# Kernel optimization log

Hardware: AMD Instinct MI355X
Metric: run time of the kernel (lower is better)

## Reference

```python
import math
import jax, jax.numpy as jnp
import numpy as np

B, S, D, H = 1, 4096, 1024, 16
HD = D // H


def setup_inputs() -> dict:
    key = jax.random.key(0)
    ks = jax.random.split(key, 11)
    s = 0.02
    inp = {
        "q": jax.random.normal(ks[0], (B, S, D), jnp.float32),
        "k": jax.random.normal(ks[1], (B, S, D), jnp.float32),
        "v": jax.random.normal(ks[2], (B, S, D), jnp.float32),
        # causal boolean mask, broadcastable over [B, H, S, S]
        "mask": jnp.tril(jnp.ones((S, S), jnp.bool_))[None, None],
        "Wq": jax.random.normal(ks[3], (D, D), jnp.float32) * s,
        "bq": jnp.zeros((D,), jnp.float32),
        "Wk": jax.random.normal(ks[4], (D, D), jnp.float32) * s,
        "bk": jnp.zeros((D,), jnp.float32),
        "Wv": jax.random.normal(ks[5], (D, D), jnp.float32) * s,
        "bv": jnp.zeros((D,), jnp.float32),
        "Wo": jax.random.normal(ks[6], (D, D), jnp.float32) * s,
        "bo": jnp.zeros((D,), jnp.float32),
    }
    return inp


def reference(q, k, v, mask, Wq, bq, Wk, bk, Wv, bv, Wo, bo):
    # projections (torch Linear: x @ W.T + b; here W is stored already transposed)
    qp = (q @ Wq + bq).reshape(B, S, H, HD)
    kp = (k @ Wk + bk).reshape(B, S, H, HD)
    vp = (v @ Wv + bv).reshape(B, S, H, HD)
    # scores: [B, H, S, S]
    scores = jnp.einsum("bqhd,bkhd->bhqk", qp, kp) / math.sqrt(HD)
    scores = jnp.where(mask, scores, -jnp.inf)
    attn = jax.nn.softmax(scores, axis=-1)
    # context: [B, H, S, HD] -> [B, S, D]
    ctx = jnp.einsum("bhqk,bkhd->bqhd", attn, vp).reshape(B, S, D)
    return ctx @ Wo + bo
```

## Files before the change

kernel.cpp:

```cpp
#include <hip/hip_runtime.h>
#include <hip/hip_bf16.h>


#define S_LEN 4096
#define D_DIM 1024
#define NHEAD 16
#define HDIM  64

typedef __hip_bfloat16 bf16;
typedef __attribute__((ext_vector_type(8))) short bf16x8v;
typedef __attribute__((ext_vector_type(4))) float f32x4;
typedef __attribute__((ext_vector_type(2))) unsigned int u32x2;

#define MFMA16(a, b, c) __builtin_amdgcn_mfma_f32_16x16x32_bf16((a), (b), (c), 0, 0, 0)

#if __has_builtin(__builtin_amdgcn_exp2f)
#define EXP2F(x) __builtin_amdgcn_exp2f(x)
#else
#define EXP2F(x) exp2f(x)
#endif

#define QSCALE (0.125f * 1.4426950408889634f)

template<int N> struct IC { static constexpr int value = N; };

__device__ __forceinline__ void async_cp16(const void* g, void* l) {
    __builtin_amdgcn_global_load_lds(
        (const __attribute__((address_space(1))) unsigned int*)g,
        (__attribute__((address_space(3))) unsigned int*)l, 16, 0, 0);
}

__device__ __forceinline__ unsigned int cvtpk_bf16(float lo, float hi) {
    unsigned int r;
    asm("v_cvt_pk_bf16_f32 %0, %1, %2" : "=v"(r) : "v"(lo), "v"(hi));
    return r;
}

__global__ __launch_bounds__(256) void cvt_bf16_k(
    const float* __restrict__ x0, const float* __restrict__ x1,
    const float* __restrict__ x2,
    bf16* __restrict__ y0, bf16* __restrict__ y1, bf16* __restrict__ y2)
{
    const float* x = (blockIdx.z == 0) ? x0 : (blockIdx.z == 1) ? x1 : x2;
    bf16*       y = (blockIdx.z == 0) ? y0 : (blockIdx.z == 1) ? y1 : y2;
    const size_t i = ((size_t)blockIdx.x * 256 + threadIdx.x);
    const float4 v = ((const float4*)x)[i];
    union { bf16 h[4]; short4 s; } u;
    u.h[0] = __float2bfloat16(v.x);
    u.h[1] = __float2bfloat16(v.y);
    u.h[2] = __float2bfloat16(v.z);
    u.h[3] = __float2bfloat16(v.w);
    ((short4*)y)[i] = u.s;
}

__global__ __launch_bounds__(256) void transpose_cvt_k(
    const float* __restrict__ W0, const float* __restrict__ W1,
    const float* __restrict__ W2, const float* __restrict__ W3,
    bf16* __restrict__ T0, bf16* __restrict__ T1,
    bf16* __restrict__ T2, bf16* __restrict__ T3)
{
    const float* W = (blockIdx.z == 0) ? W0 : (blockIdx.z == 1) ? W1
                   : (blockIdx.z == 2) ? W2 : W3;
    bf16*       Wt = (blockIdx.z == 0) ? T0 : (blockIdx.z == 1) ? T1
                   : (blockIdx.z == 2) ? T2 : T3;
    __shared__ float t[32][33];
    const int bx = blockIdx.x << 5, by = blockIdx.y << 5;
    const int tx = threadIdx.x & 31, ty = threadIdx.x >> 5;
#pragma unroll
    for (int i = 0; i < 32; i += 8)
        t[ty + i][tx] = W[(size_t)(by + ty + i) * D_DIM + bx + tx];
    __syncthreads();
#pragma unroll
    for (int i = 0; i < 32; i += 8)
        Wt[(size_t)(bx + ty + i) * D_DIM + by + tx] = __float2bfloat16(t[tx][ty + i]);
}

struct GemmJob {
    const bf16* A; const bf16* Wt; const float* bias; void* out;
    int mode; float scale;
};

__global__ __launch_bounds__(256) void gemm_k(GemmJob j0, GemmJob j1, GemmJob j2)
{
    const GemmJob j = (blockIdx.z == 0) ? j0 : (blockIdx.z == 1) ? j1 : j2;
    const int K = D_DIM;

    const int nx  = gridDim.x;
    const int lin = blockIdx.y * nx + blockIdx.x;
    const int per = (nx * gridDim.y) >> 3;
    const int bmn = (lin & 7) * per + (lin >> 3);
    const int bn = (bmn % nx) << 6;
    const int bm = (bmn / nx) << 7;

    const int tid = threadIdx.x;
    const int w = tid >> 6, lane = tid & 63;
    const int col = lane & 15, g = lane >> 4;
    const int wr = (w >> 1) << 6, wc = (w & 1) << 5;

    __shared__ bf16 As[2][128 * 64];
    __shared__ bf16 Bs[2][64 * 64];

    f32x4 acc[4][2];
#pragma unroll
    for (int i = 0; i < 4; ++i)
#pragma unroll
        for (int jj = 0; jj < 2; ++jj) acc[i][jj] = (f32x4){0.f, 0.f, 0.f, 0.f};

    auto stage = [&](int buf, int kb) {
#pragma unroll
        for (int e = 0; e < 4; ++e) {
            const int l2 = (e << 8) + tid;
            const int row = l2 >> 3, kc = l2 & 7;
            async_cp16(j.A + (size_t)(bm + row) * K + kb + (kc << 3), &As[buf][l2 << 3]);
        }
#pragma unroll
        for (int e = 0; e < 2; ++e) {
            const int l2 = (e << 8) + tid;
            const int row = l2 >> 3, kc = l2 & 7;
            async_cp16(j.Wt + (size_t)(bn + row) * K + kb + (kc << 3), &Bs[buf][l2 << 3]);
        }
    };

    stage(0, 0);
    __syncthreads();
    int cur = 0;

    for (int kb = 0; kb < K; kb += 64) {
        if (kb + 64 < K) stage(cur ^ 1, kb + 64);

#pragma unroll
        for (int s = 0; s < 2; ++s) {
            bf16x8v af[4], bfv[2];
#pragma unroll
            for (int i = 0; i < 4; ++i)
                af[i] = *(const bf16x8v*)&As[cur][((wr + (i << 4) + col) << 6) + (s << 5) + (g << 3)];
#pragma unroll
            for (int jj = 0; jj < 2; ++jj)
                bfv[jj] = *(const bf16x8v*)&Bs[cur][((wc + (jj << 4) + col) << 6) + (s << 5) + (g << 3)];
#pragma unroll
            for (int i = 0; i < 4; ++i)
#pragma unroll
                for (int jj = 0; jj < 2; ++jj)
                    acc[i][jj] = MFMA16(af[i], bfv[jj], acc[i][jj]);
        }

        __syncthreads();
        cur ^= 1;
    }

#pragma unroll
    for (int i = 0; i < 4; ++i)
#pragma unroll
    for (int jj = 0; jj < 2; ++jj)
#pragma unroll
    for (int reg = 0; reg < 4; ++reg) {
        const int row = bm + wr + (i << 4) + (g << 2) + reg;
        const int cg  = bn + wc + (jj << 4) + col;
        const float vv = (acc[i][jj][reg] + j.bias[cg]) * j.scale;
        if (j.mode == 0)
            ((bf16*)j.out)[(((size_t)(cg >> 6)) * S_LEN + row) * HDIM + (cg & 63)] =
                __float2bfloat16(vv);
        else if (j.mode == 2)
            ((bf16*)j.out)[((size_t)(cg >> 6) * HDIM + (cg & 63)) * S_LEN + row] =
                __float2bfloat16(vv);
        else
            ((float*)j.out)[(size_t)row * D_DIM + cg] = vv;
    }
}

__global__ __launch_bounds__(256) void attn_mfma_k(
    const bf16* __restrict__ Qp, const bf16* __restrict__ Kp,
    const bf16* __restrict__ Vt, bf16* __restrict__ ctx,
    float* __restrict__ Opart, float* __restrict__ lpart, int mode)
{
    __shared__ bf16 Ks[2][4096];
    __shared__ bf16 Vs[2][4096];

    const int bid = blockIdx.x;
    const int h   = bid & 15;
    const int jid = bid >> 4;

    int qb, t0, nt, chunk;
    bool dosplit, hdiag;
    if (mode == 1) {
        if (jid < 16)      { qb = 31 - jid;        t0 = 2*qb - 30; nt = 32;        dosplit = true;  chunk = 1; hdiag = true;  }
        else if (jid < 32) { qb = 31 - (jid - 16); t0 = 0;         nt = 2*qb - 30; dosplit = true;  chunk = 0; hdiag = false; }
        else               { qb = 15 - (jid - 32); t0 = 0;         nt = 2*qb + 2;  dosplit = false; chunk = 0; hdiag = true;  }
    } else {
        qb = 31 - jid; t0 = 0; nt = 2*qb + 2; dosplit = false; chunk = 0; hdiag = true;
    }

    const int q0  = qb << 7;
    const int tid = threadIdx.x, w = tid >> 6, lane = tid & 63;
    const int col = lane & 15, g = lane >> 4;

    const bf16* Kh = Kp + (size_t)h * S_LEN * HDIM;
    const bf16* Vh = Vt + (size_t)h * HDIM * S_LEN;

    const int qrowA = q0 + (w << 4) + col;
    const int qrowB = qrowA + 64;
    const size_t qbaseA = ((size_t)h * S_LEN + qrowA) * HDIM + (g << 3);
    const size_t qbaseB = qbaseA + (size_t)64 * HDIM;
    const bf16x8v qfA0 = *(const bf16x8v*)(Qp + qbaseA);
    const bf16x8v qfA1 = *(const bf16x8v*)(Qp + qbaseA + 32);
    const bf16x8v qfB0 = *(const bf16x8v*)(Qp + qbaseB);
    const bf16x8v qfB1 = *(const bf16x8v*)(Qp + qbaseB + 32);

    float plA = 0.f, plB = 0.f;
    f32x4 accA[4], accB[4];
#pragma unroll
    for (int t = 0; t < 4; ++t) {
        accA[t] = (f32x4){0.f, 0.f, 0.f, 0.f};
        accB[t] = (f32x4){0.f, 0.f, 0.f, 0.f};
    }

    auto stage = [&](int buf, int kb) {
        const int kk0 = kb << 6;
#pragma unroll
        for (int e = 0; e < 2; ++e) {
            const int lin = (e << 8) + tid;
            const int t = lin >> 7, G = (lin >> 4) & 7, c = lin & 15;
            async_cp16(Kh + (size_t)(kk0 + (t << 4) + c) * HDIM + (G << 3),
                       &Ks[buf][lin << 3]);
            async_cp16(Vh + (size_t)((t << 4) + c) * S_LEN + kk0 + (G << 3),
                       &Vs[buf][lin << 3]);
        }
    };

    auto body = [&](auto mtag, int kb, int cur) {
        constexpr int MODE = decltype(mtag)::value;
        const int kk0 = kb << 6;
        const bf16* Kc = Ks[cur];
        const bf16* Vc = Vs[cur];

        f32x4 saA[4], saB[4];
#pragma unroll
        for (int t = 0; t < 4; ++t) {
            saA[t] = (f32x4){0.f, 0.f, 0.f, 0.f};
            saB[t] = (f32x4){0.f, 0.f, 0.f, 0.f};
        }
        __builtin_amdgcn_s_setprio(1);
#pragma unroll
        for (int t = 0; t < 4; ++t) {
            const bf16x8v kf0 = *(const bf16x8v*)&Kc[((t << 7) + (g << 4) + col) << 3];
            const bf16x8v kf1 = *(const bf16x8v*)&Kc[((t << 7) + 64 + (g << 4) + col) << 3];
            if (MODE != 2) {
                saA[t] = MFMA16(kf0, qfA0, saA[t]);
                saA[t] = MFMA16(kf1, qfA1, saA[t]);
            }
            saB[t] = MFMA16(kf0, qfB0, saB[t]);
            saB[t] = MFMA16(kf1, qfB1, saB[t]);
        }
        __builtin_amdgcn_s_setprio(0);

#pragma unroll
        for (int t = 0; t < 4; ++t) {
#pragma unroll
            for (int reg = 0; reg < 4; ++reg) {
                const int kidx = kk0 + (t << 4) + (g << 2) + reg;
                if (MODE != 2) {
                    float pA;
                    if (MODE == 1 && kidx > qrowA) pA = 0.f;
                    else                           pA = EXP2F(saA[t][reg]);
                    plA += pA; saA[t][reg] = pA;
                }
                float pB;
                if (MODE == 2 && kidx > qrowB) pB = 0.f;
                else                           pB = EXP2F(saB[t][reg]);
                plB += pB; saB[t][reg] = pB;
            }
        }

        union { unsigned int wd[4]; bf16x8v v; } pA0, pA1, pB0, pB1;
        if (MODE != 2) {
            unsigned int c0[4], c1[4];
#pragma unroll
            for (int t = 0; t < 4; ++t) {
                c0[t] = cvtpk_bf16(saA[t][0], saA[t][1]);
                c1[t] = cvtpk_bf16(saA[t][2], saA[t][3]);
            }
            u32x2 r0 = __builtin_amdgcn_permlane32_swap(c0[0], c0[1], false, false);
            u32x2 r1 = __builtin_amdgcn_permlane32_swap(c1[0], c1[1], false, false);
            u32x2 s0 = __builtin_amdgcn_permlane16_swap(r0[0], r0[1], false, false);
            u32x2 s1 = __builtin_amdgcn_permlane16_swap(r1[0], r1[1], false, false);
            pA0.wd[0] = s0[0]; pA0.wd[1] = s1[0]; pA0.wd[2] = s0[1]; pA0.wd[3] = s1[1];
            r0 = __builtin_amdgcn_permlane32_swap(c0[2], c0[3], false, false);
            r1 = __builtin_amdgcn_permlane32_swap(c1[2], c1[3], false, false);
            s0 = __builtin_amdgcn_permlane16_swap(r0[0], r0[1], false, false);
            s1 = __builtin_amdgcn_permlane16_swap(r1[0], r1[1], false, false);
            pA1.wd[0] = s0[0]; pA1.wd[1] = s1[0]; pA1.wd[2] = s0[1]; pA1.wd[3] = s1[1];
        }
        {
            unsigned int c0[4], c1[4];
#pragma unroll
            for (int t = 0; t < 4; ++t) {
                c0[t] = cvtpk_bf16(saB[t][0], saB[t][1]);
                c1[t] = cvtpk_bf16(saB[t][2], saB[t][3]);
            }
            u32x2 r0 = __builtin_amdgcn_permlane32_swap(c0[0], c0[1], false, false);
            u32x2 r1 = __builtin_amdgcn_permlane32_swap(c1[0], c1[1], false, false);
            u32x2 s0 = __builtin_amdgcn_permlane16_swap(r0[0], r0[1], false, false);
            u32x2 s1 = __builtin_amdgcn_permlane16_swap(r1[0], r1[1], false, false);
            pB0.wd[0] = s0[0]; pB0.wd[1] = s1[0]; pB0.wd[2] = s0[1]; pB0.wd[3] = s1[1];
            r0 = __builtin_amdgcn_permlane32_swap(c0[2], c0[3], false, false);
            r1 = __builtin_amdgcn_permlane32_swap(c1[2], c1[3], false, false);
            s0 = __builtin_amdgcn_permlane16_swap(r0[0], r0[1], false, false);
            s1 = __builtin_amdgcn_permlane16_swap(r1[0], r1[1], false, false);
            pB1.wd[0] = s0[0]; pB1.wd[1] = s1[0]; pB1.wd[2] = s0[1]; pB1.wd[3] = s1[1];
        }

        __builtin_amdgcn_s_setprio(1);
#pragma unroll
        for (int t = 0; t < 4; ++t) {
            const bf16x8v vf0 = *(const bf16x8v*)&Vc[((t << 7) + (g << 4) + col) << 3];
            const bf16x8v vf1 = *(const bf16x8v*)&Vc[((t << 7) + 64 + (g << 4) + col) << 3];
            if (MODE != 2) {
                accA[t] = MFMA16(vf0, pA0.v, accA[t]);
                accA[t] = MFMA16(vf1, pA1.v, accA[t]);
            }
            accB[t] = MFMA16(vf0, pB0.v, accB[t]);
            accB[t] = MFMA16(vf1, pB1.v, accB[t]);
        }
        __builtin_amdgcn_s_setprio(0);
    };

    int kb = t0, cur = 0;
    const int kend = t0 + nt;
    stage(0, kb);
    __syncthreads();

    const int nmain = hdiag ? nt - 2 : nt;
    for (int i = 0; i < nmain; ++i, ++kb) {
        if (kb + 1 < kend) stage(cur ^ 1, kb + 1);
        body(IC<0>{}, kb, cur);
        __syncthreads();
        cur ^= 1;
    }
    if (hdiag) {
        stage(cur ^ 1, kb + 1);
        body(IC<1>{}, kb, cur);
        __syncthreads();
        cur ^= 1; ++kb;
        body(IC<2>{}, kb, cur);
    }

    float lA = plA, lB = plB;
    lA += __shfl_xor(lA, 16); lA += __shfl_xor(lA, 32);
    lB += __shfl_xor(lB, 16); lB += __shfl_xor(lB, 32);

    if (!dosplit) {
        const float invA = 1.f / lA;
        const float invB = 1.f / lB;
#pragma unroll
        for (int t = 0; t < 4; ++t) {
            union { bf16 hh[4]; short4 s4; } uA, uB;
#pragma unroll
            for (int reg = 0; reg < 4; ++reg) {
                uA.hh[reg] = __float2bfloat16(accA[t][reg] * invA);
                uB.hh[reg] = __float2bfloat16(accB[t][reg] * invB);
            }
            *(short4*)&ctx[(size_t)qrowA * D_DIM + h * HDIM + (t << 4) + (g << 2)] = uA.s4;
            *(short4*)&ctx[(size_t)qrowB * D_DIM + h * HDIM + (t << 4) + (g << 2)] = uB.s4;
        }
    } else {
        const int srowA = ((qb - 16) << 7) + (w << 4) + col;
        const int srowB = srowA + 64;
        float* OpA = Opart + (((size_t)chunk * NHEAD + h) * 2048 + srowA) * HDIM;
        float* OpB = Opart + (((size_t)chunk * NHEAD + h) * 2048 + srowB) * HDIM;
#pragma unroll
        for (int t = 0; t < 4; ++t) {
            *(f32x4*)&OpA[(t << 4) + (g << 2)] = accA[t];
            *(f32x4*)&OpB[(t << 4) + (g << 2)] = accB[t];
        }
        if (g == 0) {
            lpart[((size_t)chunk * NHEAD + h) * 2048 + srowA] = lA;
            lpart[((size_t)chunk * NHEAD + h) * 2048 + srowB] = lB;
        }
    }
}

__global__ __launch_bounds__(256) void combine_k(
    const float* __restrict__ Opart, const float* __restrict__ lpart,
    bf16* __restrict__ ctx)
{
    const int tid = threadIdx.x;
    const int row = (blockIdx.x << 4) + (tid >> 4);
    const int d4  = (tid & 15) << 2;
    const int h   = row >> 11;
    const int srow = row & 2047;
    const float4 a = *(const float4*)&Opart[(size_t)row * HDIM + d4];
    const float4 b = *(const float4*)&Opart[(size_t)(32768 + row) * HDIM + d4];
    const float inv = 1.f / (lpart[row] + lpart[32768 + row]);
    union { bf16 hh[4]; short4 s4; } u;
    u.hh[0] = __float2bfloat16((a.x + b.x) * inv);
    u.hh[1] = __float2bfloat16((a.y + b.y) * inv);
    u.hh[2] = __float2bfloat16((a.z + b.z) * inv);
    u.hh[3] = __float2bfloat16((a.w + b.w) * inv);
    const int qrow = 2048 + srow;
    *(short4*)&ctx[(size_t)qrow * D_DIM + h * HDIM + d4] = u.s4;
}

extern "C" void kernel_launch(void* const* d_in, const int* in_sizes, int n_in,
                              void* d_out, int out_size, void* d_ws, size_t ws_size,
                              hipStream_t stream)
{
    const float* q  = (const float*)d_in[0];
    const float* k  = (const float*)d_in[1];
    const float* v  = (const float*)d_in[2];
    const float* Wq = (const float*)d_in[4];
    const float* bq = (const float*)d_in[5];
    const float* Wk = (const float*)d_in[6];
    const float* bk = (const float*)d_in[7];
    const float* Wv = (const float*)d_in[8];
    const float* bv = (const float*)d_in[9];
    const float* Wo = (const float*)d_in[10];
    const float* bo = (const float*)d_in[11];

    const size_t PE  = (size_t)S_LEN * D_DIM;
    const size_t WTE = (size_t)D_DIM * D_DIM;

    const dim3 tg(32, 32, 4);
    const dim3 gg(D_DIM / 64, S_LEN / 128, 1);
    const dim3 gg3(D_DIM / 64, S_LEN / 128, 3);
    const dim3 cg((unsigned)(PE / 1024), 1, 3);

    if (ws_size >= (size_t)64 * 1024 * 1024) {
        bf16* Qb = (bf16*)d_ws;
        bf16* Kb = Qb + PE;
        bf16* Vb = Kb + PE;
        bf16* Qp = Vb + PE;
        bf16* Kp = Qp + PE;
        bf16* Vt = Kp + PE;
        bf16* Wtq = Vt + PE;
        bf16* Wtk = Wtq + WTE;
        bf16* Wtv = Wtk + WTE;
        bf16* Wto = Wtv + WTE;
        bf16* ctx = Qb;
        float* Opart = (float*)Kb;
        float* lpart = (float*)(Wto + WTE);

        transpose_cvt_k<<<tg, 256, 0, stream>>>(Wq, Wk, Wv, Wo, Wtq, Wtk, Wtv, Wto);
        cvt_bf16_k<<<cg, 256, 0, stream>>>(q, k, v, Qb, Kb, Vb);

        GemmJob jq{Qb, Wtq, bq, Qp, 0, QSCALE};
        GemmJob jk{Kb, Wtk, bk, Kp, 0, 1.0f};
        GemmJob jv{Vb, Wtv, bv, Vt, 2, 1.0f};
        gemm_k<<<gg3, 256, 0, stream>>>(jq, jk, jv);

        attn_mfma_k<<<dim3(768), 256, 0, stream>>>(Qp, Kp, Vt, ctx, Opart, lpart, 1);
        combine_k<<<dim3(2048), 256, 0, stream>>>(Opart, lpart, ctx);

        GemmJob jo{ctx, Wto, bo, d_out, 1, 1.0f};
        gemm_k<<<gg, 256, 0, stream>>>(jo, jo, jo);
    } else {
        bf16* X  = (bf16*)d_ws;
        bf16* Qp = X + PE;
        bf16* Kp = Qp + PE;
        bf16* Vt = Kp + PE;
        bf16* Wtq = Vt + PE;
        bf16* Wtk = Wtq + WTE;
        bf16* Wtv = Wtk + WTE;
        bf16* Wto = Wtv + WTE;

        transpose_cvt_k<<<tg, 256, 0, stream>>>(Wq, Wk, Wv, Wo, Wtq, Wtk, Wtv, Wto);

        const dim3 cg1((unsigned)(PE / 1024), 1, 1);
        cvt_bf16_k<<<cg1, 256, 0, stream>>>(q, q, q, X, X, X);
        GemmJob jq{X, Wtq, bq, Qp, 0, QSCALE};
        gemm_k<<<gg, 256, 0, stream>>>(jq, jq, jq);
        cvt_bf16_k<<<cg1, 256, 0, stream>>>(k, k, k, X, X, X);
        GemmJob jk{X, Wtk, bk, Kp, 0, 1.0f};
        gemm_k<<<gg, 256, 0, stream>>>(jk, jk, jk);
        cvt_bf16_k<<<cg1, 256, 0, stream>>>(v, v, v, X, X, X);
        GemmJob jv{X, Wtv, bv, Vt, 2, 1.0f};
        gemm_k<<<gg, 256, 0, stream>>>(jv, jv, jv);

        attn_mfma_k<<<dim3(512), 256, 0, stream>>>(Qp, Kp, Vt, X, nullptr, nullptr, 0);

        GemmJob jo{X, Wto, bo, d_out, 1, 1.0f};
        gemm_k<<<gg, 256, 0, stream>>>(jo, jo, jo);
    }
}
```

Baseline: 307.3 us.

## Swizzle GEMM shared-memory tiles and single-buffer attention K/V staging

The GEMM kernel now XOR-swizzles the 16-byte k-chunks of its A and B shared-memory tiles by row, which targets LDS bank conflicts on the MFMA fragment reads. The attention kernel drops double buffering of K/V tiles in favour of one buffer, with a load and barrier before each block and a barrier after it. This halves attention LDS use, which could allow more blocks per CU, but it removes the overlap between global loads and compute. Several variables in the host launcher are also renamed.

After: 292.5 us. 4.8% less time.

```diff
diff --git a/kernel.cpp b/kernel.cpp
--- a/kernel.cpp
+++ b/kernel.cpp
@@ -96,6 +96,7 @@
     const int w = tid >> 6, lane = tid & 63;
     const int col = lane & 15, g = lane >> 4;
     const int wr = (w >> 1) << 6, wc = (w & 1) << 5;
+    const int c7 = col & 7;
 
     __shared__ bf16 As[2][128 * 64];
     __shared__ bf16 Bs[2][64 * 64];
@@ -111,13 +112,15 @@
         for (int e = 0; e < 4; ++e) {
             const int l2 = (e << 8) + tid;
             const int row = l2 >> 3, kc = l2 & 7;
-            async_cp16(j.A + (size_t)(bm + row) * K + kb + (kc << 3), &As[buf][l2 << 3]);
+            async_cp16(j.A + (size_t)(bm + row) * K + kb + ((kc ^ (row & 7)) << 3),
+                       &As[buf][l2 << 3]);
         }
 #pragma unroll
         for (int e = 0; e < 2; ++e) {
             const int l2 = (e << 8) + tid;
             const int row = l2 >> 3, kc = l2 & 7;
-            async_cp16(j.Wt + (size_t)(bn + row) * K + kb + (kc << 3), &Bs[buf][l2 << 3]);
+            async_cp16(j.Wt + (size_t)(bn + row) * K + kb + ((kc ^ (row & 7)) << 3),
+                       &Bs[buf][l2 << 3]);
         }
     };
 
@@ -130,13 +133,14 @@
 
 #pragma unroll
         for (int s = 0; s < 2; ++s) {
+            const int gsw = (((s << 2) + g) ^ c7) << 3;
             bf16x8v af[4], bfv[2];
 #pragma unroll
             for (int i = 0; i < 4; ++i)
-                af[i] = *(const bf16x8v*)&As[cur][((wr + (i << 4) + col) << 6) + (s << 5) + (g << 3)];
+                af[i] = *(const bf16x8v*)&As[cur][((wr + (i << 4) + col) << 6) + gsw];
 #pragma unroll
             for (int jj = 0; jj < 2; ++jj)
-                bfv[jj] = *(const bf16x8v*)&Bs[cur][((wc + (jj << 4) + col) << 6) + (s << 5) + (g << 3)];
+                bfv[jj] = *(const bf16x8v*)&Bs[cur][((wc + (jj << 4) + col) << 6) + gsw];
 #pragma unroll
             for (int i = 0; i < 4; ++i)
 #pragma unroll
@@ -173,8 +177,8 @@
     const bf16* __restrict__ Vt, bf16* __restrict__ ctx,
     float* __restrict__ Opart, float* __restrict__ lpart, int mode)
 {
-    __shared__ bf16 Ks[2][4096];
-    __shared__ bf16 Vs[2][4096];
+    __shared__ bf16 Ks[4096];
+    __shared__ bf16 Vs[4096];
 
     const int bid = blockIdx.x;
     const int h   = bid & 15;
@@ -190,10 +194,10 @@
         qb = 31 - jid; t0 = 0; nt = 2*qb + 2; dosplit = false; chunk = 0; hdiag = true;
     }
 
-    const int q0  = qb << 7;
     const int tid = threadIdx.x, w = tid >> 6, lane = tid & 63;
     const int col = lane & 15, g = lane >> 4;
 
+    const int q0 = qb << 7;
     const bf16* Kh = Kp + (size_t)h * S_LEN * HDIM;
     const bf16* Vh = Vt + (size_t)h * HDIM * S_LEN;
 
@@ -214,24 +218,22 @@
         accB[t] = (f32x4){0.f, 0.f, 0.f, 0.f};
     }
 
-    auto stage = [&](int buf, int kb) {
+    auto stage = [&](int kb) {
         const int kk0 = kb << 6;
 #pragma unroll
         for (int e = 0; e < 2; ++e) {
             const int lin = (e << 8) + tid;
             const int t = lin >> 7, G = (lin >> 4) & 7, c = lin & 15;
             async_cp16(Kh + (size_t)(kk0 + (t << 4) + c) * HDIM + (G << 3),
-                       &Ks[buf][lin << 3]);
+                       &Ks[lin << 3]);
             async_cp16(Vh + (size_t)((t << 4) + c) * S_LEN + kk0 + (G << 3),
-                       &Vs[buf][lin << 3]);
+                       &Vs[lin << 3]);
         }
     };
 
-    auto body = [&](auto mtag, int kb, int cur) {
+    auto body = [&](auto mtag, int kb) {
         constexpr int MODE = decltype(mtag)::value;
         const int kk0 = kb << 6;
-        const bf16* Kc = Ks[cur];
-        const bf16* Vc = Vs[cur];
 
         f32x4 saA[4], saB[4];
 #pragma unroll
@@ -242,8 +244,8 @@
         __builtin_amdgcn_s_setprio(1);
 #pragma unroll
         for (int t = 0; t < 4; ++t) {
-            const bf16x8v kf0 = *(const bf16x8v*)&Kc[((t << 7) + (g << 4) + col) << 3];
-            const bf16x8v kf1 = *(const bf16x8v*)&Kc[((t << 7) + 64 + (g << 4) + col) << 3];
+            const bf16x8v kf0 = *(const bf16x8v*)&Ks[((t << 7) + (g << 4) + col) << 3];
+            const bf16x8v kf1 = *(const bf16x8v*)&Ks[((t << 7) + 64 + (g << 4) + col) << 3];
             if (MODE != 2) {
                 saA[t] = MFMA16(kf0, qfA0, saA[t]);
                 saA[t] = MFMA16(kf1, qfA1, saA[t]);
@@ -312,8 +314,8 @@
         __builtin_amdgcn_s_setprio(1);
 #pragma unroll
         for (int t = 0; t < 4; ++t) {
-            const bf16x8v vf0 = *(const bf16x8v*)&Vc[((t << 7) + (g << 4) + col) << 3];
-            const bf16x8v vf1 = *(const bf16x8v*)&Vc[((t << 7) + 64 + (g << 4) + col) << 3];
+            const bf16x8v vf0 = *(const bf16x8v*)&Vs[((t << 7) + (g << 4) + col) << 3];
+            const bf16x8v vf1 = *(const bf16x8v*)&Vs[((t << 7) + 64 + (g << 4) + col) << 3];
             if (MODE != 2) {
                 accA[t] = MFMA16(vf0, pA0.v, accA[t]);
                 accA[t] = MFMA16(vf1, pA1.v, accA[t]);
@@ -324,24 +326,23 @@
         __builtin_amdgcn_s_setprio(0);
     };
 
-    int kb = t0, cur = 0;
-    const int kend = t0 + nt;
-    stage(0, kb);
-    __syncthreads();
-
+    int kb = t0;
     const int nmain = hdiag ? nt - 2 : nt;
     for (int i = 0; i < nmain; ++i, ++kb) {
-        if (kb + 1 < kend) stage(cur ^ 1, kb + 1);
-        body(IC<0>{}, kb, cur);
-        __syncthreads();
-        cur ^= 1;
+        stage(kb);
+        __syncthreads();
+        body(IC<0>{}, kb);
+        __syncthreads();
     }
     if (hdiag) {
-        stage(cur ^ 1, kb + 1);
-        body(IC<1>{}, kb, cur);
-        __syncthreads();
-        cur ^= 1; ++kb;
-        body(IC<2>{}, kb, cur);
+        stage(kb);
+        __syncthreads();
+        body(IC<1>{}, kb);
+        __syncthreads();
+        ++kb;
+        stage(kb);
+        __syncthreads();
+        body(IC<2>{}, kb);
     }
 
     float lA = plA, lB = plB;
@@ -442,16 +443,16 @@
         transpose_cvt_k<<<tg, 256, 0, stream>>>(Wq, Wk, Wv, Wo, Wtq, Wtk, Wtv, Wto);
         cvt_bf16_k<<<cg, 256, 0, stream>>>(q, k, v, Qb, Kb, Vb);
 
-        GemmJob jq{Qb, Wtq, bq, Qp, 0, QSCALE};
-        GemmJob jk{Kb, Wtk, bk, Kp, 0, 1.0f};
-        GemmJob jv{Vb, Wtv, bv, Vt, 2, 1.0f};
-        gemm_k<<<gg3, 256, 0, stream>>>(jq, jk, jv);
+        GemmJob jqj{Qb, Wtq, bq, Qp, 0, QSCALE};
+        GemmJob jkj{Kb, Wtk, bk, Kp, 0, 1.0f};
+        GemmJob jvj{Vb, Wtv, bv, Vt, 2, 1.0f};
+        gemm_k<<<gg3, 256, 0, stream>>>(jqj, jkj, jvj);
 
         attn_mfma_k<<<dim3(768), 256, 0, stream>>>(Qp, Kp, Vt, ctx, Opart, lpart, 1);
         combine_k<<<dim3(2048), 256, 0, stream>>>(Opart, lpart, ctx);
 
-        GemmJob jo{ctx, Wto, bo, d_out, 1, 1.0f};
-        gemm_k<<<gg, 256, 0, stream>>>(jo, jo, jo);
+        GemmJob joj{ctx, Wto, bo, d_out, 1, 1.0f};
+        gemm_k<<<gg, 256, 0, stream>>>(joj, joj, joj);
     } else {
         bf16* X  = (bf16*)d_ws;
         bf16* Qp = X + PE;
@@ -466,18 +467,18 @@
 
         const dim3 cg1((unsigned)(PE / 1024), 1, 1);
         cvt_bf16_k<<<cg1, 256, 0, stream>>>(q, q, q, X, X, X);
-        GemmJob jq{X, Wtq, bq, Qp, 0, QSCALE};
-        gemm_k<<<gg, 256, 0, stream>>>(jq, jq, jq);
+        GemmJob jqj{X, Wtq, bq, Qp, 0, QSCALE};
+        gemm_k<<<gg, 256, 0, stream>>>(jqj, jqj, jqj);
         cvt_bf16_k<<<cg1, 256, 0, stream>>>(k, k, k, X, X, X);
-        GemmJob jk{X, Wtk, bk, Kp, 0, 1.0f};
-        gemm_k<<<gg, 256, 0, stream>>>(jk, jk, jk);
+        GemmJob jkj{X, Wtk, bk, Kp, 0, 1.0f};
+        gemm_k<<<gg, 256, 0, stream>>>(jkj, jkj, jkj);
         cvt_bf16_k<<<cg1, 256, 0, stream>>>(v, v, v, X, X, X);
-        GemmJob jv{X, Wtv, bv, Vt, 2, 1.0f};
-        gemm_k<<<gg, 256, 0, stream>>>(jv, jv, jv);
+        GemmJob jvj{X, Wtv, bv, Vt, 2, 1.0f};
+        gemm_k<<<gg, 256, 0, stream>>>(jvj, jvj, jvj);
 
         attn_mfma_k<<<dim3(512), 256, 0, stream>>>(Qp, Kp, Vt, X, nullptr, nullptr, 0);
 
-        GemmJob jo{X, Wto, bo, d_out, 1, 1.0f};
-        gemm_k<<<gg, 256, 0, stream>>>(jo, jo, jo);
-    }
-}
+        GemmJob joj{X, Wto, bo, d_out, 1, 1.0f};
+        gemm_k<<<gg, 256, 0, stream>>>(joj, joj, joj);
+    }
+}
```
